# Kernel tuning notes

Measured on AMD Instinct MI355X. Metric: run time of the kernel, lower is better.

Reference implementation:

```python
import jax, jax.numpy as jnp
import numpy as np


def setup_inputs() -> dict:
    key = jax.random.key(0)
    k0, k1, k2, k3 = jax.random.split(key, 4)
    T, H, I, E, K = 2048, 2048, 1408, 8, 2  # tokens, hidden, intermediate, experts, top-k
    hidden_states = jax.random.normal(k0, (T, H), dtype=jnp.float32)
    router_weight = jax.random.normal(k1, (H, E), dtype=jnp.float32) * 0.02
    gate_up_weight = jax.random.normal(k2, (E, H, 2 * I), dtype=jnp.float32) * 0.02
    down_weight = jax.random.normal(k3, (E, I, H), dtype=jnp.float32) * 0.02
    return {
        "hidden_states": hidden_states,
        "router_weight": router_weight,
        "gate_up_weight": gate_up_weight,
        "down_weight": down_weight,
        "top_k": K,
    }


def reference(hidden_states, router_weight, gate_up_weight, down_weight, top_k):
    # Router: logits -> softmax -> top-k -> renormalize ('normalization' path)
    router_logits = hidden_states @ router_weight                  # [T, E]
    router_weights = jax.nn.softmax(router_logits, axis=-1)       # [T, E]
    topk_w, topk_idx = jax.lax.top_k(router_weights, top_k)       # [T, K]
    topk_w = topk_w / jnp.sum(topk_w, axis=-1, keepdims=True)     # router_weights_topk_reduced

    T, H = hidden_states.shape
    I = down_weight.shape[1]

    # Grouped gate_up GEMM (dense-per-expert reference for the grouped GMM)
    gate_up = jnp.einsum('th,ehf->etf', hidden_states, gate_up_weight)  # [E, T, 2I]
    gate, up = gate_up[..., :I], gate_up[..., I:]
    swish_out = jax.nn.silu(gate) * up                              # SWIGLU  [E, T, I]
    mlp_out = jnp.einsum('eti,eih->eth', swish_out, down_weight)    # [E, T, H]

    # Scatter-combine: gather each token's top-k expert outputs, weighted sum
    sel = mlp_out[topk_idx, jnp.arange(T)[:, None]]                 # [T, K, H]
    out = jnp.sum(sel * topk_w[..., None], axis=1)                  # [T, H]
    return out
```

## Files before the change

kernel.cpp:

```cpp
#include <hip/hip_runtime.h>
#include <hip/hip_bf16.h>
#include <math.h>

#define T_TOK 2048
#define HDIM  2048
#define IDIM  1408
#define NG    2816
#define NEXP  8
#define NPAIR (T_TOK*2)
#define RPAD  6144

typedef __attribute__((ext_vector_type(4))) float  f32x4;
typedef __attribute__((ext_vector_type(4))) short  s16x4;
typedef __attribute__((ext_vector_type(8))) short  s16x8;
typedef __attribute__((ext_vector_type(8))) __bf16 bf16x8;

__device__ __forceinline__ short f2bf(float f) {
  union { float f; unsigned u; } v; v.f = f;
  unsigned r = v.u + 0x7FFFu + ((v.u >> 16) & 1u);
  return (short)(r >> 16);
}

__device__ __forceinline__ float bf2f(short s) {
  union { unsigned u; float f; } v; v.u = ((unsigned)(unsigned short)s) << 16;
  return v.f;
}

__device__ __forceinline__ void gload_lds16(const void* g, void* l) {
  __builtin_amdgcn_global_load_lds((const __attribute__((address_space(1))) unsigned int*)g,
                                   (__attribute__((address_space(3))) unsigned int*)l,
                                   16, 0, 0);
}

__global__ void router_kernel(const float* __restrict__ hs, const float* __restrict__ rw,
                              int* __restrict__ pair_e, float* __restrict__ pair_w,
                              int* __restrict__ pair_pos, int* __restrict__ counts) {
  int wid = threadIdx.x >> 6, lane = threadIdx.x & 63;
  int t = blockIdx.x * 4 + wid;
  float acc[NEXP];
#pragma unroll
  for (int e = 0; e < NEXP; e++) acc[e] = 0.f;
  const float* h = hs + (size_t)t * HDIM;
  for (int k = lane; k < HDIM; k += 64) {
    float x = h[k];
    f32x4 w0 = *(const f32x4*)(rw + (size_t)k * NEXP);
    f32x4 w1 = *(const f32x4*)(rw + (size_t)k * NEXP + 4);
#pragma unroll
    for (int e = 0; e < 4; e++) { acc[e] += x * w0[e]; acc[e + 4] += x * w1[e]; }
  }
#pragma unroll
  for (int e = 0; e < NEXP; e++)
#pragma unroll
    for (int off = 32; off > 0; off >>= 1)
      acc[e] += __shfl_xor(acc[e], off, 64);
  if (lane == 0) {
    int i1 = 0; float v1 = acc[0];
#pragma unroll
    for (int e = 1; e < NEXP; e++) if (acc[e] > v1) { v1 = acc[e]; i1 = e; }
    int i2 = -1; float v2 = -3.4e38f;
#pragma unroll
    for (int e = 0; e < NEXP; e++) if (e != i1 && acc[e] > v2) { v2 = acc[e]; i2 = e; }
    float w2 = 1.f / (1.f + expf(v1 - v2));
    float w1 = 1.f - w2;
    int p1 = atomicAdd(&counts[i1], 1);
    int p2 = atomicAdd(&counts[i2], 1);
    pair_e[2*t]   = i1; pair_w[2*t]   = w1; pair_pos[2*t]   = p1;
    pair_e[2*t+1] = i2; pair_w[2*t+1] = w2; pair_pos[2*t+1] = p2;
  }
}

__global__ void prefix_kernel(const int* __restrict__ counts, int* __restrict__ offs) {
  if (threadIdx.x == 0) {
    int s = 0;
    for (int e = 0; e < NEXP; e++) { offs[e] = s; s += (counts[e] + 255) & ~255; }
    offs[NEXP] = s;
  }
}

__global__ void rowmap_kernel(const int* __restrict__ pair_e, const float* __restrict__ pair_w,
                              const int* __restrict__ pair_pos, const int* __restrict__ offs,
                              int* __restrict__ row_token, float* __restrict__ row_weight,
                              int* __restrict__ tok2row) {
  int p = blockIdx.x * 256 + threadIdx.x;
  if (p >= NPAIR) return;
  int e = pair_e[p];
  int row = offs[e] + pair_pos[p];
  row_token[row] = p >> 1;
  row_weight[row] = pair_w[p];
  tok2row[p] = row;
}

__global__ __launch_bounds__(256) void gather_kernel(const float* __restrict__ hs,
                                                     const int* __restrict__ row_token,
                                                     short* __restrict__ A_c) {
  int r = blockIdx.x;
  int tok = row_token[r];
  int t = threadIdx.x;
  if (tok < 0) {
    *(s16x8*)&A_c[(size_t)r * HDIM + t * 8] = (s16x8)0;
    return;
  }
  const float* src = hs + (size_t)tok * HDIM + t * 8;
  f32x4 v0 = *(const f32x4*)src;
  f32x4 v1 = *(const f32x4*)(src + 4);
  s16x8 o;
#pragma unroll
  for (int j = 0; j < 4; j++) { o[j] = f2bf(v0[j]); o[4 + j] = f2bf(v1[j]); }
  int dstg = (t & ~7) | ((t & 7) ^ (r & 7));
  *(s16x8*)&A_c[(size_t)r * HDIM + dstg * 8] = o;
}

__global__ __launch_bounds__(256) void convert_w_kernel(
    const float* __restrict__ src, short* __restrict__ dst, int K, int N) {
  int e = blockIdx.z;
  src += (size_t)e * K * N;
  dst += (size_t)e * K * N;
  int n0 = blockIdx.x * 64, k0 = blockIdx.y * 64;
  __shared__ short tile[64 * 76];
  int tid = threadIdx.x;
#pragma unroll
  for (int it = 0; it < 4; it++) {
    int s = tid + it * 256;
    int kk = s >> 4, nn = (s & 15) * 4;
    f32x4 v = *(const f32x4*)(src + (size_t)(k0 + kk) * N + n0 + nn);
    s16x4 b;
#pragma unroll
    for (int j = 0; j < 4; j++) b[j] = f2bf(v[j]);
    *(s16x4*)&tile[kk * 76 + nn] = b;
  }
  __syncthreads();
#pragma unroll
  for (int it = 0; it < 2; it++) {
    int s = tid + it * 256;
    int n = s >> 3, g = s & 7;
    int gs = g ^ (n & 7);
    s16x8 o;
#pragma unroll
    for (int j = 0; j < 8; j++) o[j] = tile[(gs * 8 + j) * 76 + n];
    *(s16x8*)&dst[(size_t)(n0 + n) * K + k0 + g * 8] = o;
  }
}

__global__ __launch_bounds__(512, 2) void gateup_kernel(
    const short* __restrict__ A_c, const short* __restrict__ W,
    const int* __restrict__ offs, short* __restrict__ S) {
  int nb = blockIdx.x;
  int rb = blockIdx.y * 256;
  if (rb >= offs[NEXP]) return;
  int e = 0;
#pragma unroll
  for (int i = 1; i < NEXP; i++) e += (rb >= offs[i]);
  const short* Wb = W + (size_t)e * NG * HDIM;
  const short* Ar = A_c + (size_t)rb * HDIM;
  const short* Bg = Wb + (size_t)(nb * 128) * HDIM;
  const short* Bu = Wb + (size_t)(IDIM + nb * 128) * HDIM;

  __shared__ short As[2][256 * 64];
  __shared__ short Bs[2][256 * 64];
  int tid = threadIdx.x, lane = tid & 63, wid = tid >> 6;
  int wm = wid >> 2, wn = wid & 3;
  int lm = lane & 15, lg = lane >> 4;

  f32x4 acc[8][4];
#pragma unroll
  for (int a = 0; a < 8; a++)
#pragma unroll
    for (int b = 0; b < 4; b++) acc[a][b] = (f32x4)0.f;

  auto STAGE = [&](int buf, int kt) {
    int k0 = kt * 64;
#pragma unroll
    for (int it = 0; it < 4; it++) {
      int idx = tid + it * 512;
      gload_lds16(Ar + (size_t)(idx >> 3) * HDIM + k0 + (idx & 7) * 8, &As[buf][idx * 8]);
    }
#pragma unroll
    for (int it = 0; it < 2; it++) {
      int idx = tid + it * 512;
      gload_lds16(Bg + (size_t)(idx >> 3) * HDIM + k0 + (idx & 7) * 8, &Bs[buf][idx * 8]);
      gload_lds16(Bu + (size_t)(idx >> 3) * HDIM + k0 + (idx & 7) * 8, &Bs[buf][8192 + idx * 8]);
    }
  };
  auto READ_A = [&](bf16x8* dst, int buf, int mih, int ks) {
#pragma unroll
    for (int mi4 = 0; mi4 < 4; mi4++) {
      int m = wm * 128 + (mih * 4 + mi4) * 16 + lm;
      dst[mi4] = *(const bf16x8*)&As[buf][m * 64 + (((ks * 4 + lg) ^ (m & 7)) * 8)];
    }
  };
  auto READ_B = [&](bf16x8* dst, int buf, int ks) {
#pragma unroll
    for (int nf = 0; nf < 4; nf++) {
      int rbq = (nf >> 1) * 128 + wn * 32 + (nf & 1) * 16 + lm;
      dst[nf] = *(const bf16x8*)&Bs[buf][rbq * 64 + (((ks * 4 + lg) ^ (rbq & 7)) * 8)];
    }
  };
  auto MFMA16 = [&](const bf16x8* a, const bf16x8* b, int mih) {
    __builtin_amdgcn_s_setprio(1);
#pragma unroll
    for (int mi4 = 0; mi4 < 4; mi4++)
#pragma unroll
      for (int nf = 0; nf < 4; nf++)
        acc[mih * 4 + mi4][nf] =
            __builtin_amdgcn_mfma_f32_16x16x32_bf16(a[mi4], b[nf], acc[mih * 4 + mi4][nf], 0, 0, 0);
    __builtin_amdgcn_s_setprio(0);
  };

  STAGE(0, 0);
  const int NT = HDIM / 64;
#pragma unroll 1
  for (int kt = 0; kt < NT; kt++) {
    int cur = kt & 1;
    bf16x8 a0[4], a1[4], b0[4], b1[4];
    if (kt + 1 < NT) {
      STAGE(cur ^ 1, kt + 1);
      asm volatile("s_waitcnt vmcnt(8)" ::: "memory");
    } else {
      asm volatile("s_waitcnt vmcnt(0)" ::: "memory");
    }
    __builtin_amdgcn_s_barrier();
    READ_A(a0, cur, 0, 0); READ_B(b0, cur, 0);
    MFMA16(a0, b0, 0);
    READ_A(a1, cur, 1, 0);
    __builtin_amdgcn_s_barrier();
    MFMA16(a1, b0, 1);
    READ_A(a0, cur, 0, 1); READ_B(b1, cur, 1);
    __builtin_amdgcn_s_barrier();
    MFMA16(a0, b1, 0);
    READ_A(a1, cur, 1, 1);
    __builtin_amdgcn_s_barrier();
    MFMA16(a1, b1, 1);
    __builtin_amdgcn_s_barrier();
  }
#pragma unroll
  for (int mi = 0; mi < 8; mi++)
#pragma unroll
    for (int nfg = 0; nfg < 2; nfg++)
#pragma unroll
      for (int j = 0; j < 4; j++) {
        int row = wm * 128 + mi * 16 + lg * 4 + j;
        int rg = rb + row;
        int scol = nb * 128 + wn * 32 + nfg * 16 + lm;
        int base = scol & ~63, o = scol & 63;
        int dc = (((o >> 3) ^ (rg & 7)) << 3) | (o & 7);
        float g = acc[mi][nfg][j], u = acc[mi][nfg + 2][j];
        float sv = (g / (1.f + expf(-g))) * u;
        S[(size_t)rg * IDIM + base + dc] = f2bf(sv);
      }
}

__global__ __launch_bounds__(512, 2) void down_kernel(
    const short* __restrict__ S, const short* __restrict__ W,
    const int* __restrict__ offs, short* __restrict__ Sout) {
  int nb = blockIdx.x;
  int rb = blockIdx.y * 256;
  if (rb >= offs[NEXP]) return;
  int e = 0;
#pragma unroll
  for (int i = 1; i < NEXP; i++) e += (rb >= offs[i]);
  const short* Ar = S + (size_t)rb * IDIM;
  const short* Bw = W + (size_t)e * HDIM * IDIM + (size_t)(nb * 256) * IDIM;

  __shared__ short As[2][256 * 64];
  __shared__ short Bs[2][256 * 64];
  int tid = threadIdx.x, lane = tid & 63, wid = tid >> 6;
  int wm = wid >> 2, wn = wid & 3;
  int lm = lane & 15, lg = lane >> 4;

  f32x4 acc[8][4];
#pragma unroll
  for (int a = 0; a < 8; a++)
#pragma unroll
    for (int b = 0; b < 4; b++) acc[a][b] = (f32x4)0.f;

  auto STAGE = [&](int buf, int kt) {
    int k0 = kt * 64;
#pragma unroll
    for (int it = 0; it < 4; it++) {
      int idx = tid + it * 512;
      gload_lds16(Ar + (size_t)(idx >> 3) * IDIM + k0 + (idx & 7) * 8, &As[buf][idx * 8]);
      gload_lds16(Bw + (size_t)(idx >> 3) * IDIM + k0 + (idx & 7) * 8, &Bs[buf][idx * 8]);
    }
  };
  auto READ_A = [&](bf16x8* dst, int buf, int mih, int ks) {
#pragma unroll
    for (int mi4 = 0; mi4 < 4; mi4++) {
      int m = wm * 128 + (mih * 4 + mi4) * 16 + lm;
      dst[mi4] = *(const bf16x8*)&As[buf][m * 64 + (((ks * 4 + lg) ^ (m & 7)) * 8)];
    }
  };
  auto READ_B = [&](bf16x8* dst, int buf, int ks) {
#pragma unroll
    for (int nf = 0; nf < 4; nf++) {
      int rbq = wn * 64 + nf * 16 + lm;
      dst[nf] = *(const bf16x8*)&Bs[buf][rbq * 64 + (((ks * 4 + lg) ^ (rbq & 7)) * 8)];
    }
  };
  auto MFMA16 = [&](const bf16x8* a, const bf16x8* b, int mih) {
    __builtin_amdgcn_s_setprio(1);
#pragma unroll
    for (int mi4 = 0; mi4 < 4; mi4++)
#pragma unroll
      for (int nf = 0; nf < 4; nf++)
        acc[mih * 4 + mi4][nf] =
            __builtin_amdgcn_mfma_f32_16x16x32_bf16(a[mi4], b[nf], acc[mih * 4 + mi4][nf], 0, 0, 0);
    __builtin_amdgcn_s_setprio(0);
  };

  STAGE(0, 0);
  const int NT = IDIM / 64;
#pragma unroll 1
  for (int kt = 0; kt < NT; kt++) {
    int cur = kt & 1;
    bf16x8 a0[4], a1[4], b0[4], b1[4];
    if (kt + 1 < NT) {
      STAGE(cur ^ 1, kt + 1);
      asm volatile("s_waitcnt vmcnt(8)" ::: "memory");
    } else {
      asm volatile("s_waitcnt vmcnt(0)" ::: "memory");
    }
    __builtin_amdgcn_s_barrier();
    READ_A(a0, cur, 0, 0); READ_B(b0, cur, 0);
    MFMA16(a0, b0, 0);
    READ_A(a1, cur, 1, 0);
    __builtin_amdgcn_s_barrier();
    MFMA16(a1, b0, 1);
    READ_A(a0, cur, 0, 1); READ_B(b1, cur, 1);
    __builtin_amdgcn_s_barrier();
    MFMA16(a0, b1, 0);
    READ_A(a1, cur, 1, 1);
    __builtin_amdgcn_s_barrier();
    MFMA16(a1, b1, 1);
    __builtin_amdgcn_s_barrier();
  }
#pragma unroll
  for (int mi = 0; mi < 8; mi++)
#pragma unroll
    for (int nf = 0; nf < 4; nf++)
#pragma unroll
      for (int j = 0; j < 4; j++) {
        int row = wm * 128 + mi * 16 + lg * 4 + j;
        int col = nb * 256 + wn * 64 + nf * 16 + lm;
        Sout[(size_t)(rb + row) * HDIM + col] = f2bf(acc[mi][nf][j]);
      }
}

__global__ __launch_bounds__(256) void combine_kernel(
    const short* __restrict__ Sout, const int* __restrict__ tok2row,
    const float* __restrict__ row_weight, float* __restrict__ out) {
  int t = blockIdx.x;
  int r1 = tok2row[2 * t], r2 = tok2row[2 * t + 1];
  float w1 = row_weight[r1], w2 = row_weight[r2];
  int c = threadIdx.x * 8;
  s16x8 a = *(const s16x8*)&Sout[(size_t)r1 * HDIM + c];
  s16x8 b = *(const s16x8*)&Sout[(size_t)r2 * HDIM + c];
  float* o = out + (size_t)t * HDIM + c;
#pragma unroll
  for (int j = 0; j < 8; j++) o[j] = w1 * bf2f(a[j]) + w2 * bf2f(b[j]);
}

extern "C" void kernel_launch(void* const* d_in, const int* in_sizes, int n_in,
                              void* d_out, int out_size, void* d_ws, size_t ws_size,
                              hipStream_t stream) {
  const float* hs  = (const float*)d_in[0];
  const float* rw  = (const float*)d_in[1];
  const float* guw = (const float*)d_in[2];
  const float* dw  = (const float*)d_in[3];
  float* out = (float*)d_out;

  char* ws = (char*)d_ws;
  size_t off = 0;
  auto take = [&](size_t b) { size_t p = off; off = (off + b + 255) & ~(size_t)255; return p; };
  size_t s_off      = take((size_t)RPAD * IDIM * 2);
  int*   counts     = (int*)(ws + take(32 * 4));
  int*   offs       = (int*)(ws + take(16 * 4));
  int*   pair_e     = (int*)(ws + take(NPAIR * 4));
  float* pair_w     = (float*)(ws + take(NPAIR * 4));
  int*   pair_pos   = (int*)(ws + take(NPAIR * 4));
  int*   row_token  = (int*)(ws + take(RPAD * 4));
  float* row_weight = (float*)(ws + take(RPAD * 4));
  int*   tok2row    = (int*)(ws + take(NPAIR * 4));
  size_t ac_off     = take((size_t)RPAD * HDIM * 2);
  size_t wg_off     = take((size_t)NEXP * NG * HDIM * 2);

  short* S    = (short*)(ws + s_off);
  short* A_c  = (short*)(ws + ac_off);
  short* Wg   = (short*)(ws + wg_off);
  short* Wd   = (short*)(ws + wg_off);
  short* Sout = (short*)(ws + wg_off + ((size_t)48 << 20));

  hipMemsetAsync(counts, 0, 32 * 4, stream);
  hipMemsetAsync(row_token, 0xFF, RPAD * 4, stream);

  router_kernel<<<T_TOK / 4, 256, 0, stream>>>(hs, rw, pair_e, pair_w, pair_pos, counts);
  prefix_kernel<<<1, 64, 0, stream>>>(counts, offs);
  rowmap_kernel<<<NPAIR / 256, 256, 0, stream>>>(pair_e, pair_w, pair_pos, offs,
                                                 row_token, row_weight, tok2row);
  gather_kernel<<<RPAD, 256, 0, stream>>>(hs, row_token, A_c);

  convert_w_kernel<<<dim3(NG / 64, HDIM / 64, NEXP), 256, 0, stream>>>(guw, Wg, HDIM, NG);
  gateup_kernel<<<dim3(11, RPAD / 256), 512, 0, stream>>>(A_c, Wg, offs, S);
  convert_w_kernel<<<dim3(HDIM / 64, IDIM / 64, NEXP), 256, 0, stream>>>(dw, Wd, IDIM, HDIM);
  down_kernel<<<dim3(8, RPAD / 256), 512, 0, stream>>>(S, Wd, offs, Sout);
  combine_kernel<<<T_TOK, 256, 0, stream>>>(Sout, tok2row, row_weight, out);
}
```

Measured before the change: 297.0 us.

## Fuse gate_up weight fp32-to-bf16 conversion into the grouped GEMM B loads

Drops the separate convert_w pass for gate_up weights. The gateup kernel now reads fp32 weights directly into registers, converts them to bf16, and writes a single swizzled LDS B buffer, prefetching the next k-tile into registers while the current one is computed. The MFMA inner loop is also restructured into two k-steps with all eight A fragments loaded at once. This saves a full write and re-read of the bf16 weight copy, at the cost of each row block re-reading and re-converting fp32 weights (twice the bytes), single-buffered B in LDS, and more register pressure.

Result: faster. 289.0 us (-2.7%).

```diff
diff --git a/kernel.cpp b/kernel.cpp
--- a/kernel.cpp
+++ b/kernel.cpp
@@ -142,7 +142,7 @@
 }
 
 __global__ __launch_bounds__(512, 2) void gateup_kernel(
-    const short* __restrict__ A_c, const short* __restrict__ W,
+    const short* __restrict__ A_c, const float* __restrict__ guw,
     const int* __restrict__ offs, short* __restrict__ S) {
   int nb = blockIdx.x;
   int rb = blockIdx.y * 256;
@@ -150,86 +150,94 @@
   int e = 0;
 #pragma unroll
   for (int i = 1; i < NEXP; i++) e += (rb >= offs[i]);
-  const short* Wb = W + (size_t)e * NG * HDIM;
+  const float* Wsrc = guw + (size_t)e * HDIM * NG;
   const short* Ar = A_c + (size_t)rb * HDIM;
-  const short* Bg = Wb + (size_t)(nb * 128) * HDIM;
-  const short* Bu = Wb + (size_t)(IDIM + nb * 128) * HDIM;
-
-  __shared__ short As[2][256 * 64];
-  __shared__ short Bs[2][256 * 64];
+
+  __shared__ short bufA[2][256 * 64];
+  __shared__ short bufB[256 * 64];
   int tid = threadIdx.x, lane = tid & 63, wid = tid >> 6;
   int wm = wid >> 2, wn = wid & 3;
   int lm = lane & 15, lg = lane >> 4;
 
+  int oct = tid >> 4, kq = tid & 15;
+  int n0 = oct * 8;
+  int col = (n0 < 128) ? (nb * 128 + n0) : (IDIM + nb * 128 + (n0 - 128));
+  const float* Bp = Wsrc + col;
+
   f32x4 acc[8][4];
 #pragma unroll
   for (int a = 0; a < 8; a++)
 #pragma unroll
     for (int b = 0; b < 4; b++) acc[a][b] = (f32x4)0.f;
 
-  auto STAGE = [&](int buf, int kt) {
+  f32x4 va[4], vb[4];
+
+  auto STAGE_A = [&](int buf, int kt) {
     int k0 = kt * 64;
 #pragma unroll
     for (int it = 0; it < 4; it++) {
       int idx = tid + it * 512;
-      gload_lds16(Ar + (size_t)(idx >> 3) * HDIM + k0 + (idx & 7) * 8, &As[buf][idx * 8]);
-    }
-#pragma unroll
-    for (int it = 0; it < 2; it++) {
-      int idx = tid + it * 512;
-      gload_lds16(Bg + (size_t)(idx >> 3) * HDIM + k0 + (idx & 7) * 8, &Bs[buf][idx * 8]);
-      gload_lds16(Bu + (size_t)(idx >> 3) * HDIM + k0 + (idx & 7) * 8, &Bs[buf][8192 + idx * 8]);
-    }
-  };
-  auto READ_A = [&](bf16x8* dst, int buf, int mih, int ks) {
-#pragma unroll
-    for (int mi4 = 0; mi4 < 4; mi4++) {
-      int m = wm * 128 + (mih * 4 + mi4) * 16 + lm;
-      dst[mi4] = *(const bf16x8*)&As[buf][m * 64 + (((ks * 4 + lg) ^ (m & 7)) * 8)];
-    }
-  };
-  auto READ_B = [&](bf16x8* dst, int buf, int ks) {
-#pragma unroll
-    for (int nf = 0; nf < 4; nf++) {
-      int rbq = (nf >> 1) * 128 + wn * 32 + (nf & 1) * 16 + lm;
-      dst[nf] = *(const bf16x8*)&Bs[buf][rbq * 64 + (((ks * 4 + lg) ^ (rbq & 7)) * 8)];
-    }
-  };
-  auto MFMA16 = [&](const bf16x8* a, const bf16x8* b, int mih) {
-    __builtin_amdgcn_s_setprio(1);
-#pragma unroll
-    for (int mi4 = 0; mi4 < 4; mi4++)
-#pragma unroll
-      for (int nf = 0; nf < 4; nf++)
-        acc[mih * 4 + mi4][nf] =
-            __builtin_amdgcn_mfma_f32_16x16x32_bf16(a[mi4], b[nf], acc[mih * 4 + mi4][nf], 0, 0, 0);
-    __builtin_amdgcn_s_setprio(0);
-  };
-
-  STAGE(0, 0);
+      gload_lds16(Ar + (size_t)(idx >> 3) * HDIM + k0 + (idx & 7) * 8, &bufA[buf][idx * 8]);
+    }
+  };
+  auto LOAD_B = [&](int kt) {
+    const float* p = Bp + (size_t)(kt * 64 + kq * 4) * NG;
+#pragma unroll
+    for (int j = 0; j < 4; j++) {
+      va[j] = *(const f32x4*)(p + (size_t)j * NG);
+      vb[j] = *(const f32x4*)(p + (size_t)j * NG + 4);
+    }
+  };
+  auto WRITE_B = [&]() {
+    int gc = kq >> 1, half = kq & 1;
+#pragma unroll
+    for (int i = 0; i < 8; i++) {
+      int n = n0 + i;
+      s16x4 w;
+#pragma unroll
+      for (int j = 0; j < 4; j++) w[j] = f2bf(i < 4 ? va[j][i] : vb[j][i - 4]);
+      *(s16x4*)&bufB[n * 64 + ((gc ^ (n & 7)) * 8) + half * 4] = w;
+    }
+  };
+
+  STAGE_A(0, 0);
+  LOAD_B(0);
   const int NT = HDIM / 64;
 #pragma unroll 1
   for (int kt = 0; kt < NT; kt++) {
     int cur = kt & 1;
-    bf16x8 a0[4], a1[4], b0[4], b1[4];
     if (kt + 1 < NT) {
-      STAGE(cur ^ 1, kt + 1);
-      asm volatile("s_waitcnt vmcnt(8)" ::: "memory");
+      STAGE_A(cur ^ 1, kt + 1);
+      asm volatile("s_waitcnt vmcnt(4)" ::: "memory");
     } else {
       asm volatile("s_waitcnt vmcnt(0)" ::: "memory");
     }
-    __builtin_amdgcn_s_barrier();
-    READ_A(a0, cur, 0, 0); READ_B(b0, cur, 0);
-    MFMA16(a0, b0, 0);
-    READ_A(a1, cur, 1, 0);
-    __builtin_amdgcn_s_barrier();
-    MFMA16(a1, b0, 1);
-    READ_A(a0, cur, 0, 1); READ_B(b1, cur, 1);
-    __builtin_amdgcn_s_barrier();
-    MFMA16(a0, b1, 0);
-    READ_A(a1, cur, 1, 1);
-    __builtin_amdgcn_s_barrier();
-    MFMA16(a1, b1, 1);
+    WRITE_B();
+    if (kt + 1 < NT) LOAD_B(kt + 1);
+    asm volatile("s_waitcnt lgkmcnt(0)" ::: "memory");
+    __builtin_amdgcn_s_barrier();
+#pragma unroll
+    for (int ks = 0; ks < 2; ks++) {
+      bf16x8 a[8], b[4];
+#pragma unroll
+      for (int mi = 0; mi < 8; mi++) {
+        int m = wm * 128 + mi * 16 + lm;
+        a[mi] = *(const bf16x8*)&bufA[cur][m * 64 + (((ks * 4 + lg) ^ (m & 7)) * 8)];
+      }
+#pragma unroll
+      for (int nf = 0; nf < 4; nf++) {
+        int n = (nf >> 1) * 128 + wn * 32 + (nf & 1) * 16 + lm;
+        b[nf] = *(const bf16x8*)&bufB[n * 64 + (((ks * 4 + lg) ^ (n & 7)) * 8)];
+      }
+      __builtin_amdgcn_s_setprio(1);
+#pragma unroll
+      for (int mi = 0; mi < 8; mi++)
+#pragma unroll
+        for (int nf = 0; nf < 4; nf++)
+          acc[mi][nf] = __builtin_amdgcn_mfma_f32_16x16x32_bf16(a[mi], b[nf], acc[mi][nf], 0, 0, 0);
+      __builtin_amdgcn_s_setprio(0);
+    }
+    asm volatile("s_waitcnt lgkmcnt(0)" ::: "memory");
     __builtin_amdgcn_s_barrier();
   }
 #pragma unroll
@@ -381,13 +389,13 @@
   float* row_weight = (float*)(ws + take(RPAD * 4));
   int*   tok2row    = (int*)(ws + take(NPAIR * 4));
   size_t ac_off     = take((size_t)RPAD * HDIM * 2);
-  size_t wg_off     = take((size_t)NEXP * NG * HDIM * 2);
+  size_t sout_off   = take((size_t)RPAD * HDIM * 2);
+  size_t wd_off     = take((size_t)NEXP * HDIM * IDIM * 2);
 
   short* S    = (short*)(ws + s_off);
   short* A_c  = (short*)(ws + ac_off);
-  short* Wg   = (short*)(ws + wg_off);
-  short* Wd   = (short*)(ws + wg_off);
-  short* Sout = (short*)(ws + wg_off + ((size_t)48 << 20));
+  short* Sout = (short*)(ws + sout_off);
+  short* Wd   = (short*)(ws + wd_off);
 
   hipMemsetAsync(counts, 0, 32 * 4, stream);
   hipMemsetAsync(row_token, 0xFF, RPAD * 4, stream);
@@ -398,8 +406,7 @@
                                                  row_token, row_weight, tok2row);
   gather_kernel<<<RPAD, 256, 0, stream>>>(hs, row_token, A_c);
 
-  convert_w_kernel<<<dim3(NG / 64, HDIM / 64, NEXP), 256, 0, stream>>>(guw, Wg, HDIM, NG);
-  gateup_kernel<<<dim3(11, RPAD / 256), 512, 0, stream>>>(A_c, Wg, offs, S);
+  gateup_kernel<<<dim3(11, RPAD / 256), 512, 0, stream>>>(A_c, guw, offs, S);
   convert_w_kernel<<<dim3(HDIM / 64, IDIM / 64, NEXP), 256, 0, stream>>>(dw, Wd, IDIM, HDIM);
   down_kernel<<<dim3(8, RPAD / 256), 512, 0, stream>>>(S, Wd, offs, Sout);
   combine_kernel<<<T_TOK, 256, 0, stream>>>(Sout, tok2row, row_weight, out);
```
